# Performance work log

Measured on AMD Instinct MI355X. Metric: run time of the kernel, lower is better.

The kernel has to match this reference:

```python
import jax, jax.numpy as jnp
import numpy as np

B, C, N = 16, 1024, 32
H, Dh = 8, 16          # num_head, dim per head
D = H * Dh             # 128, model feature dim
SCALE = 0.5


def setup_inputs() -> dict:
    key = jax.random.key(0)
    ks = jax.random.split(key, 12)
    inp = {
        "atom_query": jax.random.normal(ks[0], (B, C, D), jnp.float32),
        "atom_neighbor": jax.random.normal(ks[1], (B, C, N, D), jnp.float32),
        "local_distance": jax.random.uniform(ks[2], (B, C, N, 1), jnp.float32),
        "mask": jnp.ones((B, C, N), jnp.float32),
        # Dense params (kernel [in, out], bias [out]) as in keras Dense
        "Wq": jax.random.normal(ks[3], (D, D), jnp.float32) / np.sqrt(D),
        "bq": jnp.zeros((D,), jnp.float32),
        "Wk": jax.random.normal(ks[4], (D, D), jnp.float32) / np.sqrt(D),
        "bk": jnp.zeros((D,), jnp.float32),
        "Wv": jax.random.normal(ks[5], (D, D), jnp.float32) / np.sqrt(D),
        "bv": jnp.zeros((D,), jnp.float32),
        "Wf": jax.random.normal(ks[6], (1, D), jnp.float32),
        "bf": jnp.zeros((D,), jnp.float32),
    }
    return inp


def reference(atom_query, atom_neighbor, local_distance, mask,
              Wq, bq, Wk, bk, Wv, bv, Wf, bf):
    # distance filter with swish activation: x * sigmoid(x)
    ld = local_distance @ Wf + bf              # [B,C,N,D]
    ld = ld * jax.nn.sigmoid(ld)
    an = atom_neighbor * ld                    # distance-gated neighbors

    query = atom_query @ Wq + bq               # [B,C,D]
    k = (an @ Wk + bk).reshape(B, C, N, H, Dh)  # [B,C,N,H,d]
    v = (an @ Wv + bv).reshape(B, C, N, H, Dh)

    q = query.reshape(B, C, H, Dh) * (float(Dh) ** (-SCALE))
    energy = jnp.einsum('bchd,bcnhd->bhcn', q, k)           # [B,H,C,N]
    energy = energy + (1.0 - mask[:, None, :, :]) * (-1e9)
    attn = jax.nn.softmax(energy, axis=-1)

    ctx = jnp.einsum('bhcn,bcnhd->bcnhd', attn, v)          # per-neighbor context
    ctx = ctx * mask[:, :, :, None, None]
    ctx = ctx.reshape(B, C, N, H * Dh)
    context = jnp.sum(ctx, axis=2) + query                  # [B,C,D]
    return attn, context
```

## Files before the change

kernel.cpp:

```cpp
#include <hip/hip_runtime.h>
#include <hip/hip_fp16.h>
#include <cstdint>


#define B_ 16
#define C_ 1024
#define N_ 32
#define H_ 8
#define D_ 128
#define G_ 4
#define T_ 256

typedef unsigned short u16;
typedef unsigned int u32;
typedef __fp16 hw2 __attribute__((ext_vector_type(2)));

__device__ __forceinline__ u32 pkrtz(float a, float b) {
    hw2 r = __builtin_amdgcn_cvt_pkrtz(a, b);
    return __builtin_bit_cast(u32, r);
}
__device__ __forceinline__ float fdot2(u32 a, u32 b, float c) {
#if __has_builtin(__builtin_amdgcn_fdot2)
    return __builtin_amdgcn_fdot2(__builtin_bit_cast(hw2, a),
                                  __builtin_bit_cast(hw2, b), c, false);
#else
    float2 A = __half22float2(__builtin_bit_cast(__half2, a));
    float2 B = __half22float2(__builtin_bit_cast(__half2, b));
    return fmaf(A.y, B.y, fmaf(A.x, B.x, c));
#endif
}
__device__ __forceinline__ __half2 fma2(u32 a, u32 b, __half2 c) {
    return __hfma2(__builtin_bit_cast(__half2, a),
                   __builtin_bit_cast(__half2, b), c);
}
__device__ __forceinline__ float swishf(float x) {
    float s = __builtin_amdgcn_rcpf(1.0f + __expf(-x));
    return x * s;
}

__global__ __launch_bounds__(T_, 3)
void la_kernel(const float* __restrict__ aq_g,  const float* __restrict__ an_g,
               const float* __restrict__ dist_g, const float* __restrict__ mask_g,
               const float* __restrict__ wq_g,  const float* __restrict__ bq_g,
               const float* __restrict__ wk_g,
               const float* __restrict__ wv_g,  const float* __restrict__ bv_g,
               const float* __restrict__ wf_g,  const float* __restrict__ bfb_g,
               float* __restrict__ attn_o, float* __restrict__ ctx_o)
{
    __shared__ __align__(16) u16   s_an[G_ * N_ * 136];
    __shared__ __align__(16) u32   s_ts[G_ * H_ * 68];
    __shared__ __align__(16) float s_q[G_][H_ * 20];
    __shared__ __align__(16) float s_eat[G_][H_][33];
    __shared__ float s_dist[G_][N_];
    __shared__ float s_mask[G_][N_];
    __shared__ float s_asum[G_][H_];
    __shared__ __align__(16) float s_wf[D_];
    __shared__ __align__(16) float s_bfb[D_];

    const int tid = threadIdx.x;
    const int b   = blockIdx.x >> 8;
    const int c0  = (blockIdx.x & 255) << 2;

    const int op = tid & 63;
    const int js = tid >> 6;

    float2 wq2[32];
    #pragma unroll
    for (int i = 0; i < 32; i++)
        wq2[i] = ((const float2*)(wq_g + (size_t)(js * 32 + i) * D_))[op];

    float* s_aqf = (float*)s_eat;
    if (tid < D_) {
        s_wf[tid]  = wf_g[tid];
        s_bfb[tid] = bfb_g[tid];
        int c = tid >> 5, n = tid & 31;
        int gi = (b * C_ + c0 + c) * N_ + n;
        s_dist[c][n] = dist_g[gi];
        s_mask[c][n] = mask_g[gi];
    }
    {
        s_aqf[tid] = aq_g[(b * C_ + c0 + (tid >> 7)) * D_ + (tid & 127)];
        int i2 = tid + 256;
        s_aqf[i2] = aq_g[(b * C_ + c0 + (i2 >> 7)) * D_ + (i2 & 127)];
    }
    __syncthreads();

    {
        const float4* gan = (const float4*)(an_g + (size_t)(b * C_ + c0) * N_ * D_);
        #pragma unroll
        for (int k = 0; k < 16; k++) {
            int ci = k * T_ + tid;
            float4 v = gan[ci];
            int d4 = ci & 31, n = (ci >> 5) & 31, c = ci >> 10;
            float dist = s_dist[c][n];
            int d0 = d4 << 2;
            float4 wf = *(const float4*)&s_wf[d0];
            float4 bb = *(const float4*)&s_bfb[d0];
            float g0 = swishf(fmaf(dist, wf.x, bb.x));
            float g1 = swishf(fmaf(dist, wf.y, bb.y));
            float g2 = swishf(fmaf(dist, wf.z, bb.z));
            float g3 = swishf(fmaf(dist, wf.w, bb.w));
            u32 o0 = pkrtz(v.x * g0, v.y * g1);
            u32 o1 = pkrtz(v.z * g2, v.w * g3);
            *(uint2*)(s_an + (c * N_ + n) * 136 + d0) = make_uint2(o0, o1);
        }
    }

    {
        float acc0[G_], acc1[G_];
        #pragma unroll
        for (int c = 0; c < G_; c++) { acc0[c] = 0.f; acc1[c] = 0.f; }
        #pragma unroll
        for (int i4 = 0; i4 < 8; i4++) {
            #pragma unroll
            for (int c = 0; c < G_; c++) {
                float4 a4 = *(const float4*)&s_aqf[c * D_ + js * 32 + i4 * 4];
                float2 w0 = wq2[i4 * 4], w1 = wq2[i4 * 4 + 1];
                float2 w2 = wq2[i4 * 4 + 2], w3 = wq2[i4 * 4 + 3];
                acc0[c] = fmaf(a4.x, w0.x, acc0[c]); acc1[c] = fmaf(a4.x, w0.y, acc1[c]);
                acc0[c] = fmaf(a4.y, w1.x, acc0[c]); acc1[c] = fmaf(a4.y, w1.y, acc1[c]);
                acc0[c] = fmaf(a4.z, w2.x, acc0[c]); acc1[c] = fmaf(a4.z, w2.y, acc1[c]);
                acc0[c] = fmaf(a4.w, w3.x, acc0[c]); acc1[c] = fmaf(a4.w, w3.y, acc1[c]);
            }
        }
        float* s_part = (float*)s_ts;
        #pragma unroll
        for (int c = 0; c < G_; c++) {
            *(float2*)&s_part[(js * G_ + c) * D_ + 2 * op] = make_float2(acc0[c], acc1[c]);
        }
    }
    __syncthreads();

    {
        const float* s_part = (const float*)s_ts;
        #pragma unroll
        for (int r = 0; r < 2; r++) {
            int lin = r * 256 + tid;
            int c = lin >> 7, od = lin & 127;
            float sum = s_part[(0 * G_ + c) * D_ + od] + s_part[(1 * G_ + c) * D_ + od]
                      + s_part[(2 * G_ + c) * D_ + od] + s_part[(3 * G_ + c) * D_ + od];
            s_q[c][(od >> 4) * 20 + (od & 15)] = sum + bq_g[od];
        }
    }
    __syncthreads();

    float2 wv2[32];
    #pragma unroll
    for (int i = 0; i < 32; i++)
        wv2[i] = ((const float2*)(wv_g + (size_t)(js * 32 + i) * D_))[op];

    {
        u32* t32 = s_ts;
        int h = tid & 7, jb = tid >> 3;
        float wk[4][16];
        #pragma unroll
        for (int jj = 0; jj < 4; jj++) {
            int j = 2 * jb + (jj & 1) + (jj >> 1) * 64;
            const float4* pk = (const float4*)(wk_g + j * D_ + h * 16);
            float4 k0 = pk[0], k1 = pk[1], k2 = pk[2], k3 = pk[3];
            wk[jj][0]  = k0.x; wk[jj][1]  = k0.y; wk[jj][2]  = k0.z; wk[jj][3]  = k0.w;
            wk[jj][4]  = k1.x; wk[jj][5]  = k1.y; wk[jj][6]  = k1.z; wk[jj][7]  = k1.w;
            wk[jj][8]  = k2.x; wk[jj][9]  = k2.y; wk[jj][10] = k2.z; wk[jj][11] = k2.w;
            wk[jj][12] = k3.x; wk[jj][13] = k3.y; wk[jj][14] = k3.z; wk[jj][15] = k3.w;
        }
        #pragma unroll
        for (int c = 0; c < G_; c++) {
            const float4* pq = (const float4*)&s_q[c][h * 20];
            float4 q0 = pq[0], q1 = pq[1], q2 = pq[2], q3 = pq[3];
            float qv[16] = { q0.x, q0.y, q0.z, q0.w, q1.x, q1.y, q1.z, q1.w,
                             q2.x, q2.y, q2.z, q2.w, q3.x, q3.y, q3.z, q3.w };
            float acc[4];
            #pragma unroll
            for (int jj = 0; jj < 4; jj++) {
                float a = 0.f;
                #pragma unroll
                for (int d = 0; d < 16; d++) a = fmaf(qv[d], wk[jj][d], a);
                acc[jj] = a * 0.25f;
            }
            t32[(c * 8 + h) * 68 + jb]      = pkrtz(acc[0], acc[1]);
            t32[(c * 8 + h) * 68 + 32 + jb] = pkrtz(acc[2], acc[3]);
        }
    }
    __syncthreads();

    {
        const u32* t32 = s_ts;
        int c = tid >> 6, h = (tid >> 3) & 7, n0 = tid & 7;
        const uint4* trow = (const uint4*)(t32 + (c * 8 + h) * 68);
        float acc[4] = {0.f, 0.f, 0.f, 0.f};
        #pragma unroll
        for (int jc = 0; jc < 16; jc++) {
            uint4 t4 = trow[jc];
            #pragma unroll
            for (int r = 0; r < 4; r++) {
                int n = n0 + r * 8;
                uint4 a4 = *(const uint4*)(s_an + (c * N_ + n) * 136 + jc * 8);
                float s = acc[r];
                s = fdot2(a4.x, t4.x, s);
                s = fdot2(a4.y, t4.y, s);
                s = fdot2(a4.z, t4.z, s);
                s = fdot2(a4.w, t4.w, s);
                acc[r] = s;
            }
        }
        #pragma unroll
        for (int r = 0; r < 4; r++) {
            int n = n0 + r * 8;
            float mk = s_mask[c][n];
            s_eat[c][h][n] = acc[r] + (1.0f - mk) * (-1.0e9f);
        }
    }
    __syncthreads();

    if (tid < G_ * H_) {
        int c = tid >> 3, h = tid & 7;
        float e[N_];
        float m = -3.0e38f;
        #pragma unroll
        for (int n = 0; n < N_; n++) { e[n] = s_eat[c][h][n]; m = fmaxf(m, e[n]); }
        float sum = 0.f;
        #pragma unroll
        for (int n = 0; n < N_; n++) { float p = __expf(e[n] - m); e[n] = p; sum += p; }
        float inv = 1.0f / sum;
        u32* ampk = (u32*)&s_eat[c][h][0];
        float asum = 0.f;
        size_t off = ((size_t)(b * H_ + h) * C_ + (c0 + c)) * N_;
        #pragma unroll
        for (int n4 = 0; n4 < 8; n4++) {
            float4 w;
            w.x = e[n4 * 4]     * inv;
            w.y = e[n4 * 4 + 1] * inv;
            w.z = e[n4 * 4 + 2] * inv;
            w.w = e[n4 * 4 + 3] * inv;
            *(float4*)(attn_o + off + n4 * 4) = w;
            float am0 = w.x * s_mask[c][n4 * 4];
            float am1 = w.y * s_mask[c][n4 * 4 + 1];
            float am2 = w.z * s_mask[c][n4 * 4 + 2];
            float am3 = w.w * s_mask[c][n4 * 4 + 3];
            asum += am0 + am1 + am2 + am3;
            ampk[n4 * 4]     = pkrtz(am0, am0);
            ampk[n4 * 4 + 1] = pkrtz(am1, am1);
            ampk[n4 * 4 + 2] = pkrtz(am2, am2);
            ampk[n4 * 4 + 3] = pkrtz(am3, am3);
        }
        s_asum[c][h] = asum;
    }
    __syncthreads();

    {
        int c = tid >> 6, h = (tid >> 3) & 7, jg = tid & 7;
        const u32* ampk = (const u32*)&s_eat[c][h][0];
        __half2 acc2[8];
        #pragma unroll
        for (int i = 0; i < 8; i++) acc2[i] = __float2half2_rn(0.f);
        #pragma unroll 4
        for (int n = 0; n < N_; n++) {
            u32 am2 = ampk[n];
            const uint4* arow = (const uint4*)(s_an + (c * N_ + n) * 136 + jg * 16);
            uint4 a0 = arow[0], a1 = arow[1];
            acc2[0] = fma2(a0.x, am2, acc2[0]);
            acc2[1] = fma2(a0.y, am2, acc2[1]);
            acc2[2] = fma2(a0.z, am2, acc2[2]);
            acc2[3] = fma2(a0.w, am2, acc2[3]);
            acc2[4] = fma2(a1.x, am2, acc2[4]);
            acc2[5] = fma2(a1.y, am2, acc2[5]);
            acc2[6] = fma2(a1.z, am2, acc2[6]);
            acc2[7] = fma2(a1.w, am2, acc2[7]);
        }
        float* srow = (float*)(s_an + c * (N_ * 136)) + h * 132 + jg * 16;
        #pragma unroll
        for (int p = 0; p < 4; p++) {
            float2 lo = __half22float2(acc2[p * 2]);
            float2 hi = __half22float2(acc2[p * 2 + 1]);
            *(float4*)(srow + p * 4) = make_float4(lo.x, lo.y, hi.x, hi.y);
        }
    }
    __syncthreads();

    {
        int h = op >> 3;
        float acc0[G_], acc1[G_];
        #pragma unroll
        for (int c = 0; c < G_; c++) { acc0[c] = 0.f; acc1[c] = 0.f; }
        #pragma unroll
        for (int i4 = 0; i4 < 8; i4++) {
            #pragma unroll
            for (int c = 0; c < G_; c++) {
                const float* sc_ = (const float*)(s_an + c * (N_ * 136));
                float4 s4 = *(const float4*)&sc_[h * 132 + js * 32 + i4 * 4];
                float2 w0 = wv2[i4 * 4], w1 = wv2[i4 * 4 + 1];
                float2 w2 = wv2[i4 * 4 + 2], w3 = wv2[i4 * 4 + 3];
                acc0[c] = fmaf(s4.x, w0.x, acc0[c]); acc1[c] = fmaf(s4.x, w0.y, acc1[c]);
                acc0[c] = fmaf(s4.y, w1.x, acc0[c]); acc1[c] = fmaf(s4.y, w1.y, acc1[c]);
                acc0[c] = fmaf(s4.z, w2.x, acc0[c]); acc1[c] = fmaf(s4.z, w2.y, acc1[c]);
                acc0[c] = fmaf(s4.w, w3.x, acc0[c]); acc1[c] = fmaf(s4.w, w3.y, acc1[c]);
            }
        }
        float* s_gp = (float*)s_ts;
        #pragma unroll
        for (int c = 0; c < G_; c++) {
            *(float2*)&s_gp[(js * G_ + c) * D_ + 2 * op] = make_float2(acc0[c], acc1[c]);
        }
    }
    __syncthreads();

    {
        const float* s_gp = (const float*)s_ts;
        #pragma unroll
        for (int r = 0; r < 2; r++) {
            int lin = r * 256 + tid;
            int c = lin >> 7, od = lin & 127;
            int h = od >> 4;
            float sum = s_gp[(0 * G_ + c) * D_ + od] + s_gp[(1 * G_ + c) * D_ + od]
                      + s_gp[(2 * G_ + c) * D_ + od] + s_gp[(3 * G_ + c) * D_ + od];
            float r0 = sum + s_asum[c][h] * bv_g[od] + s_q[c][h * 20 + (od & 15)];
            ctx_o[((size_t)(b * C_ + c0 + c)) * D_ + od] = r0;
        }
    }
}

extern "C" void kernel_launch(void* const* d_in, const int* in_sizes, int n_in,
                              void* d_out, int out_size, void* d_ws, size_t ws_size,
                              hipStream_t stream) {
    const float* aq   = (const float*)d_in[0];
    const float* an   = (const float*)d_in[1];
    const float* dist = (const float*)d_in[2];
    const float* mask = (const float*)d_in[3];
    const float* wq   = (const float*)d_in[4];
    const float* bq   = (const float*)d_in[5];
    const float* wk   = (const float*)d_in[6];
    const float* wv   = (const float*)d_in[8];
    const float* bv   = (const float*)d_in[9];
    const float* wf   = (const float*)d_in[10];
    const float* bfb  = (const float*)d_in[11];

    float* attn_o = (float*)d_out;
    float* ctx_o  = attn_o + (size_t)B_ * H_ * C_ * N_;

    dim3 grid(B_ * C_ / G_), block(T_);
    hipLaunchKernelGGL(la_kernel, grid, block, 0, stream,
                       aq, an, dist, mask, wq, bq, wk, wv, bv, wf, bfb,
                       attn_o, ctx_o);
}
```

Measured before the change: 453.5 us.

## Double block threads to 512 and stream Wq/Wv weights instead of register-caching

Raises the block size from 256 to 512 threads and splits every phase's work across twice as many threads, so each thread handles fewer neighbors, columns or query rows. The Wq and Wv weight slices are no longer preloaded into 32 float2 registers per thread; they are read from global (L2-cached) memory inside the projection loops. The goal is lower register pressure and more resident waves to hide latency. The cost is more global weight loads per block and an extra barrier inside the attention-weighted accumulation phase.

```diff
diff --git a/kernel.cpp b/kernel.cpp
--- a/kernel.cpp
+++ b/kernel.cpp
@@ -9,7 +9,7 @@
 #define H_ 8
 #define D_ 128
 #define G_ 4
-#define T_ 256
+#define T_ 512
 
 typedef unsigned short u16;
 typedef unsigned int u32;
@@ -38,7 +38,7 @@
     return x * s;
 }
 
-__global__ __launch_bounds__(T_, 3)
+__global__ __launch_bounds__(T_, 6)
 void la_kernel(const float* __restrict__ aq_g,  const float* __restrict__ an_g,
                const float* __restrict__ dist_g, const float* __restrict__ mask_g,
                const float* __restrict__ wq_g,  const float* __restrict__ bq_g,
@@ -61,14 +61,6 @@
     const int b   = blockIdx.x >> 8;
     const int c0  = (blockIdx.x & 255) << 2;
 
-    const int op = tid & 63;
-    const int js = tid >> 6;
-
-    float2 wq2[32];
-    #pragma unroll
-    for (int i = 0; i < 32; i++)
-        wq2[i] = ((const float2*)(wq_g + (size_t)(js * 32 + i) * D_))[op];
-
     float* s_aqf = (float*)s_eat;
     if (tid < D_) {
         s_wf[tid]  = wf_g[tid];
@@ -78,17 +70,13 @@
         s_dist[c][n] = dist_g[gi];
         s_mask[c][n] = mask_g[gi];
     }
-    {
-        s_aqf[tid] = aq_g[(b * C_ + c0 + (tid >> 7)) * D_ + (tid & 127)];
-        int i2 = tid + 256;
-        s_aqf[i2] = aq_g[(b * C_ + c0 + (i2 >> 7)) * D_ + (i2 & 127)];
-    }
+    s_aqf[tid] = aq_g[(b * C_ + c0 + (tid >> 7)) * D_ + (tid & 127)];
     __syncthreads();
 
     {
         const float4* gan = (const float4*)(an_g + (size_t)(b * C_ + c0) * N_ * D_);
         #pragma unroll
-        for (int k = 0; k < 16; k++) {
+        for (int k = 0; k < 8; k++) {
             int ci = k * T_ + tid;
             float4 v = gan[ci];
             int d4 = ci & 31, n = (ci >> 5) & 31, c = ci >> 10;
@@ -107,55 +95,52 @@
     }
 
     {
-        float acc0[G_], acc1[G_];
-        #pragma unroll
-        for (int c = 0; c < G_; c++) { acc0[c] = 0.f; acc1[c] = 0.f; }
+        const int op  = tid & 63;
+        const int js4 = (tid >> 6) & 3;
+        const int ch  = tid >> 8;
+        const int cA  = ch * 2, cB = cA + 1;
+        float a0A = 0.f, a1A = 0.f, a0B = 0.f, a1B = 0.f;
         #pragma unroll
         for (int i4 = 0; i4 < 8; i4++) {
-            #pragma unroll
-            for (int c = 0; c < G_; c++) {
-                float4 a4 = *(const float4*)&s_aqf[c * D_ + js * 32 + i4 * 4];
-                float2 w0 = wq2[i4 * 4], w1 = wq2[i4 * 4 + 1];
-                float2 w2 = wq2[i4 * 4 + 2], w3 = wq2[i4 * 4 + 3];
-                acc0[c] = fmaf(a4.x, w0.x, acc0[c]); acc1[c] = fmaf(a4.x, w0.y, acc1[c]);
-                acc0[c] = fmaf(a4.y, w1.x, acc0[c]); acc1[c] = fmaf(a4.y, w1.y, acc1[c]);
-                acc0[c] = fmaf(a4.z, w2.x, acc0[c]); acc1[c] = fmaf(a4.z, w2.y, acc1[c]);
-                acc0[c] = fmaf(a4.w, w3.x, acc0[c]); acc1[c] = fmaf(a4.w, w3.y, acc1[c]);
-            }
+            int j = js4 * 32 + i4 * 4;
+            float2 w0 = ((const float2*)(wq_g + (size_t)(j + 0) * D_))[op];
+            float2 w1 = ((const float2*)(wq_g + (size_t)(j + 1) * D_))[op];
+            float2 w2 = ((const float2*)(wq_g + (size_t)(j + 2) * D_))[op];
+            float2 w3 = ((const float2*)(wq_g + (size_t)(j + 3) * D_))[op];
+            float4 aA = *(const float4*)&s_aqf[cA * D_ + j];
+            float4 aB = *(const float4*)&s_aqf[cB * D_ + j];
+            a0A = fmaf(aA.x, w0.x, a0A); a1A = fmaf(aA.x, w0.y, a1A);
+            a0A = fmaf(aA.y, w1.x, a0A); a1A = fmaf(aA.y, w1.y, a1A);
+            a0A = fmaf(aA.z, w2.x, a0A); a1A = fmaf(aA.z, w2.y, a1A);
+            a0A = fmaf(aA.w, w3.x, a0A); a1A = fmaf(aA.w, w3.y, a1A);
+            a0B = fmaf(aB.x, w0.x, a0B); a1B = fmaf(aB.x, w0.y, a1B);
+            a0B = fmaf(aB.y, w1.x, a0B); a1B = fmaf(aB.y, w1.y, a1B);
+            a0B = fmaf(aB.z, w2.x, a0B); a1B = fmaf(aB.z, w2.y, a1B);
+            a0B = fmaf(aB.w, w3.x, a0B); a1B = fmaf(aB.w, w3.y, a1B);
         }
         float* s_part = (float*)s_ts;
-        #pragma unroll
-        for (int c = 0; c < G_; c++) {
-            *(float2*)&s_part[(js * G_ + c) * D_ + 2 * op] = make_float2(acc0[c], acc1[c]);
-        }
+        *(float2*)&s_part[(js4 * 4 + cA) * D_ + 2 * op] = make_float2(a0A, a1A);
+        *(float2*)&s_part[(js4 * 4 + cB) * D_ + 2 * op] = make_float2(a0B, a1B);
     }
     __syncthreads();
 
     {
         const float* s_part = (const float*)s_ts;
-        #pragma unroll
-        for (int r = 0; r < 2; r++) {
-            int lin = r * 256 + tid;
-            int c = lin >> 7, od = lin & 127;
-            float sum = s_part[(0 * G_ + c) * D_ + od] + s_part[(1 * G_ + c) * D_ + od]
-                      + s_part[(2 * G_ + c) * D_ + od] + s_part[(3 * G_ + c) * D_ + od];
-            s_q[c][(od >> 4) * 20 + (od & 15)] = sum + bq_g[od];
-        }
-    }
-    __syncthreads();
-
-    float2 wv2[32];
-    #pragma unroll
-    for (int i = 0; i < 32; i++)
-        wv2[i] = ((const float2*)(wv_g + (size_t)(js * 32 + i) * D_))[op];
+        int c = tid >> 7, od = tid & 127;
+        float sum = s_part[(0 * 4 + c) * D_ + od] + s_part[(1 * 4 + c) * D_ + od]
+                  + s_part[(2 * 4 + c) * D_ + od] + s_part[(3 * 4 + c) * D_ + od];
+        s_q[c][(od >> 4) * 20 + (od & 15)] = sum + bq_g[od];
+    }
+    __syncthreads();
 
     {
         u32* t32 = s_ts;
-        int h = tid & 7, jb = tid >> 3;
-        float wk[4][16];
-        #pragma unroll
-        for (int jj = 0; jj < 4; jj++) {
-            int j = 2 * jb + (jj & 1) + (jj >> 1) * 64;
+        int h = tid & 7, a = (tid >> 3) & 31, half = tid >> 8;
+        int p = a + 32 * half;
+        float wk[2][16];
+        #pragma unroll
+        for (int jj = 0; jj < 2; jj++) {
+            int j = 2 * p + jj;
             const float4* pk = (const float4*)(wk_g + j * D_ + h * 16);
             float4 k0 = pk[0], k1 = pk[1], k2 = pk[2], k3 = pk[3];
             wk[jj][0]  = k0.x; wk[jj][1]  = k0.y; wk[jj][2]  = k0.z; wk[jj][3]  = k0.w;
@@ -167,33 +152,44 @@
         for (int c = 0; c < G_; c++) {
             const float4* pq = (const float4*)&s_q[c][h * 20];
             float4 q0 = pq[0], q1 = pq[1], q2 = pq[2], q3 = pq[3];
-            float qv[16] = { q0.x, q0.y, q0.z, q0.w, q1.x, q1.y, q1.z, q1.w,
-                             q2.x, q2.y, q2.z, q2.w, q3.x, q3.y, q3.z, q3.w };
-            float acc[4];
+            float acc[2];
             #pragma unroll
-            for (int jj = 0; jj < 4; jj++) {
-                float a = 0.f;
-                #pragma unroll
-                for (int d = 0; d < 16; d++) a = fmaf(qv[d], wk[jj][d], a);
-                acc[jj] = a * 0.25f;
+            for (int jj = 0; jj < 2; jj++) {
+                float v = 0.f;
+                v = fmaf(q0.x, wk[jj][0],  v);
+                v = fmaf(q0.y, wk[jj][1],  v);
+                v = fmaf(q0.z, wk[jj][2],  v);
+                v = fmaf(q0.w, wk[jj][3],  v);
+                v = fmaf(q1.x, wk[jj][4],  v);
+                v = fmaf(q1.y, wk[jj][5],  v);
+                v = fmaf(q1.z, wk[jj][6],  v);
+                v = fmaf(q1.w, wk[jj][7],  v);
+                v = fmaf(q2.x, wk[jj][8],  v);
+                v = fmaf(q2.y, wk[jj][9],  v);
+                v = fmaf(q2.z, wk[jj][10], v);
+                v = fmaf(q2.w, wk[jj][11], v);
+                v = fmaf(q3.x, wk[jj][12], v);
+                v = fmaf(q3.y, wk[jj][13], v);
+                v = fmaf(q3.z, wk[jj][14], v);
+                v = fmaf(q3.w, wk[jj][15], v);
+                acc[jj] = v * 0.25f;
             }
-            t32[(c * 8 + h) * 68 + jb]      = pkrtz(acc[0], acc[1]);
-            t32[(c * 8 + h) * 68 + 32 + jb] = pkrtz(acc[2], acc[3]);
+            t32[(c * 8 + h) * 68 + p] = pkrtz(acc[0], acc[1]);
         }
     }
     __syncthreads();
 
     {
         const u32* t32 = s_ts;
-        int c = tid >> 6, h = (tid >> 3) & 7, n0 = tid & 7;
+        int c = tid >> 7, h = (tid >> 4) & 7, n0 = tid & 15;
         const uint4* trow = (const uint4*)(t32 + (c * 8 + h) * 68);
-        float acc[4] = {0.f, 0.f, 0.f, 0.f};
+        float acc[2] = {0.f, 0.f};
         #pragma unroll
         for (int jc = 0; jc < 16; jc++) {
             uint4 t4 = trow[jc];
             #pragma unroll
-            for (int r = 0; r < 4; r++) {
-                int n = n0 + r * 8;
+            for (int r = 0; r < 2; r++) {
+                int n = n0 + r * 16;
                 uint4 a4 = *(const uint4*)(s_an + (c * N_ + n) * 136 + jc * 8);
                 float s = acc[r];
                 s = fdot2(a4.x, t4.x, s);
@@ -204,8 +200,8 @@
             }
         }
         #pragma unroll
-        for (int r = 0; r < 4; r++) {
-            int n = n0 + r * 8;
+        for (int r = 0; r < 2; r++) {
+            int n = n0 + r * 16;
             float mk = s_mask[c][n];
             s_eat[c][h][n] = acc[r] + (1.0f - mk) * (-1.0e9f);
         }
@@ -248,74 +244,72 @@
     __syncthreads();
 
     {
-        int c = tid >> 6, h = (tid >> 3) & 7, jg = tid & 7;
+        int c = tid >> 7, h = (tid >> 4) & 7, jg = tid & 15;
         const u32* ampk = (const u32*)&s_eat[c][h][0];
-        __half2 acc2[8];
-        #pragma unroll
-        for (int i = 0; i < 8; i++) acc2[i] = __float2half2_rn(0.f);
+        __half2 acc2[4];
+        #pragma unroll
+        for (int i = 0; i < 4; i++) acc2[i] = __float2half2_rn(0.f);
         #pragma unroll 4
         for (int n = 0; n < N_; n++) {
             u32 am2 = ampk[n];
-            const uint4* arow = (const uint4*)(s_an + (c * N_ + n) * 136 + jg * 16);
-            uint4 a0 = arow[0], a1 = arow[1];
+            uint4 a0 = *(const uint4*)(s_an + (c * N_ + n) * 136 + jg * 8);
             acc2[0] = fma2(a0.x, am2, acc2[0]);
             acc2[1] = fma2(a0.y, am2, acc2[1]);
             acc2[2] = fma2(a0.z, am2, acc2[2]);
             acc2[3] = fma2(a0.w, am2, acc2[3]);
-            acc2[4] = fma2(a1.x, am2, acc2[4]);
-            acc2[5] = fma2(a1.y, am2, acc2[5]);
-            acc2[6] = fma2(a1.z, am2, acc2[6]);
-            acc2[7] = fma2(a1.w, am2, acc2[7]);
-        }
-        float* srow = (float*)(s_an + c * (N_ * 136)) + h * 132 + jg * 16;
-        #pragma unroll
-        for (int p = 0; p < 4; p++) {
-            float2 lo = __half22float2(acc2[p * 2]);
-            float2 hi = __half22float2(acc2[p * 2 + 1]);
-            *(float4*)(srow + p * 4) = make_float4(lo.x, lo.y, hi.x, hi.y);
-        }
-    }
-    __syncthreads();
-
-    {
-        int h = op >> 3;
-        float acc0[G_], acc1[G_];
-        #pragma unroll
-        for (int c = 0; c < G_; c++) { acc0[c] = 0.f; acc1[c] = 0.f; }
+        }
+        __syncthreads();
+        float* srow = (float*)(s_an + c * (N_ * 136)) + h * 132 + jg * 8;
+        float2 f0 = __half22float2(acc2[0]);
+        float2 f1 = __half22float2(acc2[1]);
+        float2 f2 = __half22float2(acc2[2]);
+        float2 f3 = __half22float2(acc2[3]);
+        *(float4*)(srow + 0) = make_float4(f0.x, f0.y, f1.x, f1.y);
+        *(float4*)(srow + 4) = make_float4(f2.x, f2.y, f3.x, f3.y);
+    }
+    __syncthreads();
+
+    {
+        const int op  = tid & 63;
+        const int js4 = (tid >> 6) & 3;
+        const int ch  = tid >> 8;
+        const int cA  = ch * 2, cB = cA + 1;
+        const int h   = op >> 3;
+        const float* scA = (const float*)(s_an + cA * (N_ * 136));
+        const float* scB = (const float*)(s_an + cB * (N_ * 136));
+        float a0A = 0.f, a1A = 0.f, a0B = 0.f, a1B = 0.f;
         #pragma unroll
         for (int i4 = 0; i4 < 8; i4++) {
-            #pragma unroll
-            for (int c = 0; c < G_; c++) {
-                const float* sc_ = (const float*)(s_an + c * (N_ * 136));
-                float4 s4 = *(const float4*)&sc_[h * 132 + js * 32 + i4 * 4];
-                float2 w0 = wv2[i4 * 4], w1 = wv2[i4 * 4 + 1];
-                float2 w2 = wv2[i4 * 4 + 2], w3 = wv2[i4 * 4 + 3];
-                acc0[c] = fmaf(s4.x, w0.x, acc0[c]); acc1[c] = fmaf(s4.x, w0.y, acc1[c]);
-                acc0[c] = fmaf(s4.y, w1.x, acc0[c]); acc1[c] = fmaf(s4.y, w1.y, acc1[c]);
-                acc0[c] = fmaf(s4.z, w2.x, acc0[c]); acc1[c] = fmaf(s4.z, w2.y, acc1[c]);
-                acc0[c] = fmaf(s4.w, w3.x, acc0[c]); acc1[c] = fmaf(s4.w, w3.y, acc1[c]);
-            }
+            int j = js4 * 32 + i4 * 4;
+            float2 w0 = ((const float2*)(wv_g + (size_t)(j + 0) * D_))[op];
+            float2 w1 = ((const float2*)(wv_g + (size_t)(j + 1) * D_))[op];
+            float2 w2 = ((const float2*)(wv_g + (size_t)(j + 2) * D_))[op];
+            float2 w3 = ((const float2*)(wv_g + (size_t)(j + 3) * D_))[op];
+            float4 sA = *(const float4*)&scA[h * 132 + j];
+            float4 sB = *(const float4*)&scB[h * 132 + j];
+            a0A = fmaf(sA.x, w0.x, a0A); a1A = fmaf(sA.x, w0.y, a1A);
+            a0A = fmaf(sA.y, w1.x, a0A); a1A = fmaf(sA.y, w1.y, a1A);
+            a0A = fmaf(sA.z, w2.x, a0A); a1A = fmaf(sA.z, w2.y, a1A);
+            a0A = fmaf(sA.w, w3.x, a0A); a1A = fmaf(sA.w, w3.y, a1A);
+            a0B = fmaf(sB.x, w0.x, a0B); a1B = fmaf(sB.x, w0.y, a1B);
+            a0B = fmaf(sB.y, w1.x, a0B); a1B = fmaf(sB.y, w1.y, a1B);
+            a0B = fmaf(sB.z, w2.x, a0B); a1B = fmaf(sB.z, w2.y, a1B);
+            a0B = fmaf(sB.w, w3.x, a0B); a1B = fmaf(sB.w, w3.y, a1B);
         }
         float* s_gp = (float*)s_ts;
-        #pragma unroll
-        for (int c = 0; c < G_; c++) {
-            *(float2*)&s_gp[(js * G_ + c) * D_ + 2 * op] = make_float2(acc0[c], acc1[c]);
-        }
+        *(float2*)&s_gp[(js4 * 4 + cA) * D_ + 2 * op] = make_float2(a0A, a1A);
+        *(float2*)&s_gp[(js4 * 4 + cB) * D_ + 2 * op] = make_float2(a0B, a1B);
     }
     __syncthreads();
 
     {
         const float* s_gp = (const float*)s_ts;
-        #pragma unroll
-        for (int r = 0; r < 2; r++) {
-            int lin = r * 256 + tid;
-            int c = lin >> 7, od = lin & 127;
-            int h = od >> 4;
-            float sum = s_gp[(0 * G_ + c) * D_ + od] + s_gp[(1 * G_ + c) * D_ + od]
-                      + s_gp[(2 * G_ + c) * D_ + od] + s_gp[(3 * G_ + c) * D_ + od];
-            float r0 = sum + s_asum[c][h] * bv_g[od] + s_q[c][h * 20 + (od & 15)];
-            ctx_o[((size_t)(b * C_ + c0 + c)) * D_ + od] = r0;
-        }
+        int c = tid >> 7, od = tid & 127;
+        int h = od >> 4;
+        float sum = s_gp[(0 * 4 + c) * D_ + od] + s_gp[(1 * 4 + c) * D_ + od]
+                  + s_gp[(2 * 4 + c) * D_ + od] + s_gp[(3 * 4 + c) * D_ + od];
+        float r0 = sum + s_asum[c][h] * bv_g[od] + s_q[c][h * 20 + (od & 15)];
+        ctx_o[((size_t)(b * C_ + c0 + c)) * D_ + od] = r0;
     }
 }
 
```

Result: no change. 454.4 us (+0.2%).
